# Performance work log

Hardware: AMD Instinct MI355X
Metric: run time of the kernel (lower is better)

The kernel has to match this reference:

```python
import math
import jax, jax.numpy as jnp
import numpy as np

B, L, DIM, HEADS = 4, 2048, 1024, 8
HEAD = DIM // HEADS  # 128
SCALE_BASE = 512.0
EPS = 1e-5  # nn.GroupNorm default


def _xpos(x, downscale=False):
    # x: (..., L, dh). Faithful port of the RetNet XPOS (Jamie-Stirling impl).
    l, dh = x.shape[-2], x.shape[-1]
    half = dh // 2
    pos = jnp.arange(l, dtype=x.dtype)
    base = (jnp.arange(0, dh, 2, dtype=x.dtype) + 0.4 * dh) / (1.4 * dh)  # (half,)
    scale = base[None, :] ** (pos[:, None] / SCALE_BASE)                  # (L, half)
    inv_freq = 1.0 / (10000.0 ** (jnp.arange(half, dtype=x.dtype) / half))
    sinusoid = pos[:, None] * inv_freq[None, :]                           # (L, half)
    sin, cos = jnp.sin(sinusoid), jnp.cos(sinusoid)
    if downscale:
        scale = 1.0 / scale
    s = jnp.repeat(sin * scale, 2, axis=-1)  # duplicate_interleave -> (L, dh)
    c = jnp.repeat(cos * scale, 2, axis=-1)
    x1, x2 = x[..., ::2], x[..., 1::2]
    rot = jnp.stack([-x2, x1], axis=-1).reshape(x.shape)  # rotate_every_two
    return x * c + rot * s


def _decay_mask(l, gammas):
    # D[h, n, m] = gamma_h ** (n - m) for n >= m else 0
    n = jnp.arange(l)[:, None]
    m = jnp.arange(l)[None, :]
    lg = jnp.log(gammas)  # (h,)
    expo = (n - m).astype(jnp.float32)[None, :, :] * lg[:, None, None]
    return jnp.where((n >= m)[None], jnp.exp(expo), 0.0)  # (h, L, L)


def setup_inputs() -> dict:
    key = jax.random.key(0)
    ks = jax.random.split(key, 6)
    d = DIM
    return {
        "X": jax.random.normal(ks[0], (B, L, DIM), dtype=jnp.float32),
        "W_Q": jax.random.normal(ks[1], (HEADS, DIM, HEAD), dtype=jnp.float32) / d,
        "W_K": jax.random.normal(ks[2], (HEADS, DIM, HEAD), dtype=jnp.float32) / d,
        "W_V": jax.random.normal(ks[3], (HEADS, DIM, HEAD), dtype=jnp.float32) / d,
        "W_G": jax.random.normal(ks[4], (DIM, DIM), dtype=jnp.float32) / d,
        "W_O": jax.random.normal(ks[5], (DIM, DIM), dtype=jnp.float32) / d,
        "gn_weight": jnp.ones((DIM,), dtype=jnp.float32),
        "gn_bias": jnp.zeros((DIM,), dtype=jnp.float32),
    }


def reference(X, W_Q, W_K, W_V, W_G, W_O, gn_weight, gn_bias):
    b, l, d = X.shape
    h = W_Q.shape[0]
    # gammas = 1 - exp(linspace(log 1/32, log 1/512, heads))
    gammas = 1.0 - jnp.exp(jnp.linspace(math.log(1.0 / 32.0), math.log(1.0 / 512.0), h)).astype(jnp.float32)

    Q = jnp.einsum('bld,hde->bhle', X, W_Q)
    K = jnp.einsum('bld,hde->bhle', X, W_K)
    V = jnp.einsum('bld,hdv->bhlv', X, W_V)
    Q = _xpos(Q)
    K = _xpos(K, downscale=True)

    D = _decay_mask(l, gammas).astype(X.dtype)           # (h, L, L)
    scores = jnp.einsum('bhle,bhme->bhlm', Q, K) * D[None]
    Y = jnp.einsum('bhlm,bhmv->bhlv', scores, V)          # (b, h, L, head_v)

    # GroupNorm(heads, V) on rows of shape (V,): normalize per head group
    mean = Y.mean(axis=-1, keepdims=True)
    var = Y.var(axis=-1, keepdims=True)
    Yn = (Y - mean) * jax.lax.rsqrt(var + EPS)
    Yn = jnp.transpose(Yn, (0, 2, 1, 3)).reshape(b, l, -1)  # concat heads -> (b, L, V)
    Yn = Yn * gn_weight + gn_bias

    G = X @ W_G
    out = (G * jax.nn.sigmoid(G) * Yn) @ W_O  # swish gate then output proj
    return out
```

## Files before the change

### kernel.cpp

```cpp
#include <hip/hip_runtime.h>
#include <cmath>

#define BB 4
#define LL 2048
#define DD 1024
#define HH 8
#define MM (BB * LL)

struct Gammas { float lg2[8]; };
struct MMArgs { const ushort* Bt[4]; void* C[4]; void* C2[4]; int emode[4]; };

typedef __attribute__((ext_vector_type(8))) short bf16x8;
typedef __attribute__((ext_vector_type(4))) float f32x4;

__device__ __forceinline__ ushort f2bf(float f) {
    uint u = __builtin_bit_cast(uint, f);
    uint r = (u + 0x7fffu + ((u >> 16) & 1u)) >> 16;
    return (ushort)r;
}
__device__ __forceinline__ float bf2f(ushort h) {
    uint u = ((uint)h) << 16;
    return __builtin_bit_cast(float, u);
}
__device__ __forceinline__ void gload16(const void* g, void* l) {
    __builtin_amdgcn_global_load_lds((const __attribute__((address_space(1))) void*)g,
                                     (__attribute__((address_space(3))) void*)l, 16, 0, 0);
}

__global__ void xpos_table_kernel(float4* __restrict__ tbl) {
    int tid = blockIdx.x * blockDim.x + threadIdx.x;
    if (tid >= LL * 64) return;
    int l = tid >> 6, i = tid & 63;
    float inv = powf(10000.0f, -(float)i / 64.0f);
    float ang = (float)l * inv;
    float s = sinf(ang), c = cosf(ang);
    float base = (2.0f * (float)i + 51.2f) / 179.2f;
    float sc = powf(base, (float)l / 512.0f);
    tbl[tid] = make_float4(c * sc, s * sc, c / sc, s / sc);
}

__global__ __launch_bounds__(256) void cast_kernel(const float* __restrict__ X,
                                                   ushort* __restrict__ Xb) {
    int i = (blockIdx.x * 256 + threadIdx.x) * 4;
    float4 v = *(const float4*)&X[i];
    ushort4 o;
    o.x = f2bf(v.x); o.y = f2bf(v.y); o.z = f2bf(v.z); o.w = f2bf(v.w);
    *(ushort4*)&Xb[i] = o;
}

__global__ __launch_bounds__(256) void wtrans_kernel(const float* __restrict__ W,
                                                     ushort* __restrict__ Wt, int perhead) {
    __shared__ float T[64][68];
    const int k0 = blockIdx.y * 64, n0 = blockIdx.x * 64;
    const int t = threadIdx.x;
    for (int f = t; f < 64 * 16; f += 256) {
        int kk = f >> 4, s = f & 15;
        int n = n0 + s * 4;
        size_t src = perhead ? (size_t)(n >> 7) * 131072 + (size_t)(k0 + kk) * 128 + (n & 127)
                             : (size_t)(k0 + kk) * 1024 + n;
        *(float4*)&T[kk][s * 4] = *(const float4*)&W[src];
    }
    __syncthreads();
    for (int f = t; f < 64 * 8; f += 256) {
        int n = f >> 3, s = f & 7;
        __align__(16) ushort tmp[8];
        #pragma unroll
        for (int j = 0; j < 8; j++) tmp[j] = f2bf(T[s * 8 + j][n]);
        *(uint4*)&Wt[(size_t)(n0 + n) * 1024 + k0 + s * 8] = *(uint4*)tmp;
    }
}

#define MM8_STEP(T, STAGE, VM)                                                  \
  {                                                                             \
    const int buf_ = (T) & 3;                                                   \
    const int sbuf_ = ((T) + 2) & 3;                                            \
    if (STAGE) {                                                                \
      const int nk_ = ((T) + 2) * 32;                                           \
      gload16(gA0 + nk_, &As[sbuf_][ldst]);                                     \
      gload16(gA1 + nk_, &As[sbuf_][4096 + ldst]);                              \
    }                                                                           \
    asm volatile("s_waitcnt vmcnt(" #VM ")" ::: "memory");                      \
    __builtin_amdgcn_sched_barrier(0);                                          \
    __builtin_amdgcn_s_barrier();                                               \
    __builtin_amdgcn_sched_barrier(0);                                          \
    bf16x8 am[8], bn[4];                                                        \
    _Pragma("unroll")                                                           \
    for (int mi = 0; mi < 4; mi++)                                              \
      am[mi] = *(const bf16x8*)&As[buf_][aoff + mi * 512];                      \
    _Pragma("unroll")                                                           \
    for (int ni = 0; ni < 4; ni++)                                              \
      bn[ni] = *(const bf16x8*)&Bs[buf_][boff + ni * 512];                      \
    __builtin_amdgcn_s_setprio(1);                                              \
    _Pragma("unroll")                                                           \
    for (int mi = 0; mi < 4; mi++)                                              \
      _Pragma("unroll")                                                         \
      for (int ni = 0; ni < 4; ni++)                                            \
        acc[mi][ni] = __builtin_amdgcn_mfma_f32_16x16x32_bf16(                  \
            am[mi], bn[ni], acc[mi][ni], 0, 0, 0);                              \
    __builtin_amdgcn_s_setprio(0);                                              \
    __builtin_amdgcn_sched_barrier(0);                                          \
    if (STAGE) {                                                                \
      const int nk_ = ((T) + 2) * 32;                                           \
      gload16(gB0 + nk_, &Bs[sbuf_][ldst]);                                     \
      gload16(gB1 + nk_, &Bs[sbuf_][4096 + ldst]);                              \
    }                                                                           \
    __builtin_amdgcn_sched_barrier(0);                                          \
    __builtin_amdgcn_s_barrier();                                               \
    __builtin_amdgcn_sched_barrier(0);                                          \
    _Pragma("unroll")                                                           \
    for (int mi = 4; mi < 8; mi++)                                              \
      am[mi] = *(const bf16x8*)&As[buf_][aoff + mi * 512];                      \
    __builtin_amdgcn_s_setprio(1);                                              \
    _Pragma("unroll")                                                           \
    for (int mi = 4; mi < 8; mi++)                                              \
      _Pragma("unroll")                                                         \
      for (int ni = 0; ni < 4; ni++)                                            \
        acc[mi][ni] = __builtin_amdgcn_mfma_f32_16x16x32_bf16(                  \
            am[mi], bn[ni], acc[mi][ni], 0, 0, 0);                              \
    __builtin_amdgcn_s_setprio(0);                                              \
  }

__global__ __launch_bounds__(512) void mm8_kernel(
    const ushort* __restrict__ A, MMArgs args, const float4* __restrict__ tbl)
{
    __shared__ __align__(16) ushort As[4][8192];
    __shared__ __align__(16) ushort Bs[4][8192];
    const int t = threadIdx.x;
    const int w = t >> 6, lane = t & 63;
    const int ln = lane & 15, quad = lane >> 4;
    const int which = blockIdx.x >> 2;
    const ushort* Bt = args.Bt[which];
    void* Cv = args.C[which];
    void* Cv2 = args.C2[which];
    const int emode = args.emode[which];
    const int n0 = (blockIdx.x & 3) * 256, m0 = blockIdx.y * 256;
    const int wm = w & 1, wn = w >> 1;

    f32x4 acc[8][4];
    const f32x4 fzero = {0.f, 0.f, 0.f, 0.f};
    #pragma unroll
    for (int i = 0; i < 8; i++)
        #pragma unroll
        for (int j = 0; j < 4; j++) acc[i][j] = fzero;

    const int srow = w * 16 + (lane >> 2);
    const int scol = ((lane & 3) ^ ((lane >> 3) & 3)) * 8;
    const ushort* gA0 = A  + (size_t)(m0 + srow) * 1024 + scol;
    const ushort* gA1 = gA0 + (size_t)128 * 1024;
    const ushort* gB0 = Bt + (size_t)(n0 + srow) * 1024 + scol;
    const ushort* gB1 = gB0 + (size_t)128 * 1024;
    const int ldst = w * 512;

    const int cQ = (quad ^ ((ln >> 1) & 3)) * 8;
    const int aoff = (wm * 128 + ln) * 32 + cQ;
    const int boff = (wn * 64 + ln) * 32 + cQ;

    #pragma unroll
    for (int tt = 0; tt < 2; ++tt) {
        gload16(gA0 + tt * 32, &As[tt][ldst]);
        gload16(gA1 + tt * 32, &As[tt][4096 + ldst]);
        gload16(gB0 + tt * 32, &Bs[tt][ldst]);
        gload16(gB1 + tt * 32, &Bs[tt][4096 + ldst]);
    }

    for (int T = 0; T < 30; ++T) {
        MM8_STEP(T, 1, 6);
    }
    MM8_STEP(30, 0, 4);
    MM8_STEP(31, 0, 0);

    #pragma unroll
    for (int mi = 0; mi < 8; mi++) {
        #pragma unroll
        for (int ni = 0; ni < 4; ni++) {
            const int row0 = m0 + wm * 128 + mi * 16 + quad * 4;
            const int e = wn * 64 + ni * 16 + ln;
            const int col = n0 + e;
            if (emode == 5) {
                const int b = row0 >> 11, l0 = row0 & (LL - 1);
                ushort4 pk;
                pk.x = f2bf(acc[mi][ni][0]); pk.y = f2bf(acc[mi][ni][1]);
                pk.z = f2bf(acc[mi][ni][2]); pk.w = f2bf(acc[mi][ni][3]);
                *(ushort4*)&((ushort*)Cv)[((size_t)(b * 1024 + col)) * 2048 + l0] = pk;
                continue;
            }
            float vv[4];
            #pragma unroll
            for (int r = 0; r < 4; r++) {
                float v = acc[mi][ni][r];
                if (emode == 1 || emode == 2 || emode == 6) {
                    float4 tt = tbl[(size_t)((row0 + r) & (LL - 1)) * 64 + ((col & 127) >> 1)];
                    float cc = (emode == 1) ? tt.x : tt.z;
                    float ss = (emode == 1) ? tt.y : tt.w;
                    float partner = __shfl_xor(v, 1);
                    float rot = (col & 1) ? partner : -partner;
                    v = v * cc + rot * ss;
                } else if (emode == 3) {
                    v = v / (1.0f + expf(-v));
                }
                vv[r] = v;
                if (emode == 4)
                    ((float*)Cv)[(size_t)(row0 + r) * 1024 + col] = v;
                else
                    ((ushort*)Cv)[(size_t)(row0 + r) * 1024 + col] = f2bf(v);
            }
            if (emode == 6) {
                const int b = row0 >> 11, l0 = row0 & (LL - 1);
                ushort4 pk;
                pk.x = f2bf(vv[0]); pk.y = f2bf(vv[1]);
                pk.z = f2bf(vv[2]); pk.w = f2bf(vv[3]);
                *(ushort4*)&((ushort*)Cv2)[((size_t)(b * 1024 + col)) * 2048 + l0] = pk;
            }
        }
    }
}

__global__ __launch_bounds__(256) void mm_kernel(
    const ushort* __restrict__ A, MMArgs args, const float4* __restrict__ tbl)
{
    __shared__ __align__(16) ushort As[2][128 * 32];
    __shared__ __align__(16) ushort Bs[2][128 * 32];
    const int t = threadIdx.x;
    const int w = t >> 6, lane = t & 63;
    const int ln = lane & 15, quad = lane >> 4;
    const int which = blockIdx.x >> 3;
    const ushort* Bt = args.Bt[which];
    void* Cv = args.C[which];
    const int emode = args.emode[which];
    const int n0 = (blockIdx.x & 7) * 128, m0 = blockIdx.y * 128;
    const int wm = w & 1, wn = w >> 1;

    f32x4 acc[4][4];
    const f32x4 fzero = {0.f, 0.f, 0.f, 0.f};
    #pragma unroll
    for (int i = 0; i < 4; i++)
        #pragma unroll
        for (int j = 0; j < 4; j++) acc[i][j] = fzero;

    const int srow = w * 32 + (lane >> 2);
    const int scol = (lane & 3) * 8;
    const ushort* ga  = A  + (size_t)(m0 + srow) * 1024 + scol;
    const ushort* ga2 = ga + 16 * 1024;
    const ushort* gb  = Bt + (size_t)(n0 + srow) * 1024 + scol;
    const ushort* gb2 = gb + 16 * 1024;
    const int lo1 = (w * 32) * 32;
    const int lo2 = (w * 32 + 16) * 32;

    gload16(ga, &As[0][lo1]);
    gload16(ga2, &As[0][lo2]);
    gload16(gb, &Bs[0][lo1]);
    gload16(gb2, &Bs[0][lo2]);
    __syncthreads();

    for (int kt = 0; kt < 1024; kt += 32) {
        const int cur = (kt >> 5) & 1;
        if (kt < 1024 - 32) {
            const int nk = kt + 32;
            gload16(ga + nk, &As[cur ^ 1][lo1]);
            gload16(ga2 + nk, &As[cur ^ 1][lo2]);
            gload16(gb + nk, &Bs[cur ^ 1][lo1]);
            gload16(gb2 + nk, &Bs[cur ^ 1][lo2]);
        }
        bf16x8 am[4], bn[4];
        #pragma unroll
        for (int i = 0; i < 4; i++)
            am[i] = *(const bf16x8*)&As[cur][(wm * 64 + i * 16 + ln) * 32 + quad * 8];
        #pragma unroll
        for (int i = 0; i < 4; i++)
            bn[i] = *(const bf16x8*)&Bs[cur][(wn * 64 + i * 16 + ln) * 32 + quad * 8];
        #pragma unroll
        for (int mi = 0; mi < 4; mi++)
            #pragma unroll
            for (int ni = 0; ni < 4; ni++)
                acc[mi][ni] = __builtin_amdgcn_mfma_f32_16x16x32_bf16(
                    am[mi], bn[ni], acc[mi][ni], 0, 0, 0);
        __syncthreads();
    }

    #pragma unroll
    for (int mi = 0; mi < 4; mi++) {
        #pragma unroll
        for (int ni = 0; ni < 4; ni++) {
            const int row0 = m0 + wm * 64 + mi * 16 + quad * 4;
            const int e = wn * 64 + ni * 16 + ln;
            const int col = n0 + e;
            #pragma unroll
            for (int r = 0; r < 4; r++) {
                float v = acc[mi][ni][r];
                if (emode == 3) v = v / (1.0f + expf(-v));
                if (emode == 4)
                    ((float*)Cv)[(size_t)(row0 + r) * 1024 + col] = v;
                else
                    ((ushort*)Cv)[(size_t)(row0 + r) * 1024 + col] = f2bf(v);
            }
        }
    }
}

__global__ __launch_bounds__(256) void state_kernel(
    const ushort* __restrict__ Ktb, const ushort* __restrict__ Vt,
    ushort* __restrict__ Sb, Gammas gp)
{
    __shared__ __align__(16) ushort shbuf[2 * 128 * 72];
    ushort* Ktl = shbuf;
    ushort* Vwl = shbuf + 128 * 72;

    const int t = threadIdx.x;
    const int w = t >> 6, lane = t & 63, ln = lane & 15, quad = lane >> 4;
    const int c = blockIdx.x, bh = blockIdx.y;
    const int b = bh >> 3, h = bh & 7;
    const float lg2 = gp.lg2[h];
    const size_t tbase = ((size_t)b * 1024 + h * 128) * 2048 + (size_t)c * 64;

    const int sr = t >> 1, soff = (t & 1) * 32;
    #pragma unroll
    for (int j = 0; j < 4; j++)
        *(uint4*)&Ktl[sr * 72 + soff + j * 8] =
            *(const uint4*)&Ktb[tbase + (size_t)sr * 2048 + soff + j * 8];
    #pragma unroll
    for (int j = 0; j < 4; j++) {
        uint4 raw = *(const uint4*)&Vt[tbase + (size_t)sr * 2048 + soff + j * 8];
        ushort* rp = (ushort*)&raw;
        __align__(16) ushort tmp[8];
        #pragma unroll
        for (int jj = 0; jj < 8; jj++) {
            int m = soff + j * 8 + jj;
            tmp[jj] = f2bf(bf2f(rp[jj]) * exp2f(lg2 * (float)(63 - m)));
        }
        *(uint4*)&Vwl[sr * 72 + soff + j * 8] = *(uint4*)tmp;
    }
    __syncthreads();

    const int wm = w & 1, wn = w >> 1;
    f32x4 acc[4][4];
    const f32x4 fzero = {0.f, 0.f, 0.f, 0.f};
    #pragma unroll
    for (int i = 0; i < 4; i++)
        #pragma unroll
        for (int j = 0; j < 4; j++) acc[i][j] = fzero;

    #pragma unroll
    for (int ks = 0; ks < 2; ks++) {
        bf16x8 am[4], bn[4];
        #pragma unroll
        for (int mi = 0; mi < 4; mi++)
            am[mi] = *(const bf16x8*)&Ktl[(wm * 64 + mi * 16 + ln) * 72 + ks * 32 + quad * 8];
        #pragma unroll
        for (int ni = 0; ni < 4; ni++)
            bn[ni] = *(const bf16x8*)&Vwl[(wn * 64 + ni * 16 + ln) * 72 + ks * 32 + quad * 8];
        #pragma unroll
        for (int mi = 0; mi < 4; mi++)
            #pragma unroll
            for (int ni = 0; ni < 4; ni++)
                acc[mi][ni] = __builtin_amdgcn_mfma_f32_16x16x32_bf16(
                    am[mi], bn[ni], acc[mi][ni], 0, 0, 0);
    }
    __syncthreads();

    ushort* Lsh = shbuf;
    #pragma unroll
    for (int mi = 0; mi < 4; mi++) {
        #pragma unroll
        for (int ni = 0; ni < 4; ni++) {
            const int d0 = wm * 64 + mi * 16 + quad * 4;
            const int v = wn * 64 + ni * 16 + ln;
            ushort4 pk;
            pk.x = f2bf(acc[mi][ni][0]); pk.y = f2bf(acc[mi][ni][1]);
            pk.z = f2bf(acc[mi][ni][2]); pk.w = f2bf(acc[mi][ni][3]);
            *(ushort4*)&Lsh[v * 136 + d0] = pk;
        }
    }
    __syncthreads();
    ushort* dst = Sb + (size_t)(bh * 32 + c) * 128 * 128;
    const int orow = t >> 1, ooff = (t & 1) * 64;
    #pragma unroll
    for (int j = 0; j < 8; j++)
        *(uint4*)&dst[(size_t)orow * 128 + ooff + j * 8] =
            *(uint4*)&Lsh[orow * 136 + ooff + j * 8];
}

__global__ __launch_bounds__(256) void scan_kernel(ushort* __restrict__ Sb, Gammas gp)
{
    const int t = threadIdx.x;
    const int vb = blockIdx.x, bh = blockIdx.y;
    const int h = bh & 7;
    const float g64 = exp2f(64.0f * gp.lg2[h]);
    const int v = vb * 16 + (t >> 4);
    const int d0 = (t & 15) * 8;

    float acc[8];
    #pragma unroll
    for (int j = 0; j < 8; j++) acc[j] = 0.f;

    for (int c = 1; c < 32; c++) {
        ushort* p = Sb + ((size_t)(bh * 32 + (c - 1)) * 128 + v) * 128 + d0;
        uint4 lv = *(const uint4*)p;
        ushort* lp = (ushort*)&lv;
        __align__(16) ushort o[8];
        #pragma unroll
        for (int j = 0; j < 8; j++) {
            acc[j] = g64 * acc[j] + bf2f(lp[j]);
            o[j] = f2bf(acc[j]);
        }
        *(uint4*)p = *(uint4*)o;
    }
}

__global__ __launch_bounds__(256) void ret2_kernel(
    const ushort* __restrict__ Qb, const ushort* __restrict__ Kb,
    const ushort* __restrict__ Vt, const ushort* __restrict__ Pt,
    const ushort* __restrict__ Gb,
    const float* __restrict__ gnw, const float* __restrict__ gnb,
    ushort* __restrict__ Z, Gammas gp)
{
    __shared__ __align__(16) ushort Ks[64 * 136];
    __shared__ __align__(16) ushort Vs[128 * 72];
    __shared__ __align__(16) ushort Ss[64 * 72];
    __shared__ __align__(16) ushort Ps[128 * 136];

    const int t = threadIdx.x;
    const int w = t >> 6, lane = t & 63, ln = lane & 15, quad = lane >> 4;
    const int c = blockIdx.x, bh = blockIdx.y;
    const int b = bh >> 3, h = bh & 7;
    const float lg2 = gp.lg2[h];
    const size_t qkbase = (size_t)b * LL * 1024 + (size_t)h * 128;
    const size_t vtbase = ((size_t)b * 1024 + h * 128) * 2048;
    const int n0 = c * 64;

    float dmk[4], drr[4];
    #pragma unroll
    for (int kt = 0; kt < 4; kt++)
        dmk[kt] = exp2f(-(float)(kt * 16 + quad * 4) * lg2);
    #pragma unroll
    for (int r = 0; r < 4; r++)
        drr[r] = exp2f(-(float)r * lg2);

    float gwv[8], gbv[8];
    #pragma unroll
    for (int vt = 0; vt < 8; vt++) {
        gwv[vt] = gnw[h * 128 + vt * 16 + ln];
        gbv[vt] = gnb[h * 128 + vt * 16 + ln];
    }

    const int krow = t >> 4, kc = (t & 15) * 8;
    const int vrow = t >> 3, vc = (t & 7) * 8;
    #pragma unroll
    for (int i = 0; i < 4; i++)
        *(uint4*)&Ks[(krow + i * 16) * 136 + kc] =
            *(const uint4*)&Kb[qkbase + (size_t)(n0 + krow + i * 16) * 1024 + kc];
    #pragma unroll
    for (int i = 0; i < 4; i++)
        *(uint4*)&Vs[(vrow + i * 32) * 72 + vc] =
            *(const uint4*)&Vt[vtbase + (size_t)(vrow + i * 32) * 2048 + n0 + vc];
    if (c > 0) {
        const ushort* psrc = Pt + (size_t)(bh * 32 + (c - 1)) * 128 * 128;
        const int pr = t >> 1, poff = (t & 1) * 64;
        #pragma unroll
        for (int j = 0; j < 8; j++)
            *(uint4*)&Ps[pr * 136 + poff + j * 8] =
                *(const uint4*)&psrc[(size_t)pr * 128 + poff + j * 8];
    }

    bf16x8 aq[4];
    #pragma unroll
    for (int ks = 0; ks < 4; ks++)
        aq[ks] = *(const bf16x8*)&Qb[qkbase + (size_t)(n0 + 16 * w + ln) * 1024
                                     + ks * 32 + quad * 8];
    f32x4 y[8];
    const f32x4 fzero = {0.f, 0.f, 0.f, 0.f};
    #pragma unroll
    for (int vt = 0; vt < 8; vt++) y[vt] = fzero;

    __syncthreads();

    if (c > 0) {
        #pragma unroll
        for (int ks = 0; ks < 4; ks++) {
            #pragma unroll
            for (int vt = 0; vt < 8; vt++) {
                bf16x8 bp = *(const bf16x8*)&Ps[(vt * 16 + ln) * 136 + ks * 32 + quad * 8];
                y[vt] = __builtin_amdgcn_mfma_f32_16x16x32_bf16(aq[ks], bp, y[vt], 0, 0, 0);
            }
        }
        #pragma unroll
        for (int rr = 0; rr < 4; rr++) {
            const float sc = exp2f(lg2 * (float)(16 * w + quad * 4 + rr + 1));
            #pragma unroll
            for (int vt = 0; vt < 8; vt++) y[vt][rr] *= sc;
        }
    }

    f32x4 s4[4];
    #pragma unroll
    for (int kt = 0; kt < 4; kt++) s4[kt] = fzero;
    #pragma unroll
    for (int ks = 0; ks < 4; ks++) {
        #pragma unroll
        for (int kt = 0; kt < 4; kt++) {
            bf16x8 bk = *(const bf16x8*)&Ks[(kt * 16 + ln) * 136 + ks * 32 + quad * 8];
            s4[kt] = __builtin_amdgcn_mfma_f32_16x16x32_bf16(bk, aq[ks], s4[kt], 0, 0, 0);
        }
    }
    const float dq = exp2f((float)(16 * w + ln) * lg2);
    #pragma unroll
    for (int kt = 0; kt < 4; kt++) {
        const float db = dq * dmk[kt];
        ushort4 pk;
        pk.x = f2bf((kt * 16 + quad * 4 + 0 <= 16 * w + ln) ? s4[kt][0] * db * drr[0] : 0.f);
        pk.y = f2bf((kt * 16 + quad * 4 + 1 <= 16 * w + ln) ? s4[kt][1] * db * drr[1] : 0.f);
        pk.z = f2bf((kt * 16 + quad * 4 + 2 <= 16 * w + ln) ? s4[kt][2] * db * drr[2] : 0.f);
        pk.w = f2bf((kt * 16 + quad * 4 + 3 <= 16 * w + ln) ? s4[kt][3] * db * drr[3] : 0.f);
        *(ushort4*)&Ss[(16 * w + ln) * 72 + kt * 16 + quad * 4] = pk;
    }
    #pragma unroll
    for (int ks2 = 0; ks2 < 2; ks2++) {
        bf16x8 as = *(const bf16x8*)&Ss[(16 * w + ln) * 72 + ks2 * 32 + quad * 8];
        #pragma unroll
        for (int vt = 0; vt < 8; vt++) {
            bf16x8 bv = *(const bf16x8*)&Vs[(vt * 16 + ln) * 72 + ks2 * 32 + quad * 8];
            y[vt] = __builtin_amdgcn_mfma_f32_16x16x32_bf16(as, bv, y[vt], 0, 0, 0);
        }
    }

    #pragma unroll
    for (int r = 0; r < 4; r++) {
        float s = 0.f, sq = 0.f;
        #pragma unroll
        for (int vt = 0; vt < 8; vt++) {
            float v = y[vt][r];
            s += v; sq += v * v;
        }
        #pragma unroll
        for (int off = 8; off >= 1; off >>= 1) {
            s  += __shfl_xor(s, off, 64);
            sq += __shfl_xor(sq, off, 64);
        }
        float mean = s * 0.0078125f;
        float var = sq * 0.0078125f - mean * mean;
        float rstd = rsqrtf(var + 1e-5f);
        const size_t row = (size_t)(b * LL + n0 + 16 * w + quad * 4 + r);
        #pragma unroll
        for (int vt = 0; vt < 8; vt++) {
            float gv = bf2f(Gb[row * 1024 + h * 128 + vt * 16 + ln]);
            float o = (y[vt][r] - mean) * rstd * gwv[vt] + gbv[vt];
            Z[row * 1024 + h * 128 + vt * 16 + ln] = f2bf(o * gv);
        }
    }
}

extern "C" void kernel_launch(void* const* d_in, const int* in_sizes, int n_in,
                              void* d_out, int out_size, void* d_ws, size_t ws_size,
                              hipStream_t stream) {
    const float* X   = (const float*)d_in[0];
    const float* Wq  = (const float*)d_in[1];
    const float* Wk  = (const float*)d_in[2];
    const float* Wv  = (const float*)d_in[3];
    const float* Wg  = (const float*)d_in[4];
    const float* Wo  = (const float*)d_in[5];
    const float* gnw = (const float*)d_in[6];
    const float* gnb = (const float*)d_in[7];
    float* out = (float*)d_out;

    const size_t MB = 1u << 20;
    char* base = (char*)d_ws;
    ushort* Sb  = (ushort*)base;
    float4* tbl = (float4*)base;
    ushort* Xb  = (ushort*)(base + 2 * MB);
    ushort* Wqt = (ushort*)(base + 18 * MB);
    ushort* Wkt = (ushort*)(base + 20 * MB);
    ushort* Wvt = (ushort*)(base + 22 * MB);
    ushort* Wgt = (ushort*)(base + 24 * MB);
    ushort* Wot = (ushort*)(base + 32 * MB);
    ushort* Qb  = (ushort*)(base + 34 * MB);
    ushort* Kb  = (ushort*)(base + 50 * MB);
    ushort* Gb  = (ushort*)(base + 66 * MB);
    ushort* Vt  = (ushort*)(base + 82 * MB);
    ushort* Ktb = (ushort*)(base + 98 * MB);
    ushort* Zb  = (ushort*)(base + 98 * MB);

    Gammas gp;
    for (int h = 0; h < 8; h++) {
        double lin = log(1.0 / 32.0) +
                     (log(1.0 / 512.0) - log(1.0 / 32.0)) * (double)h / 7.0;
        float gamma = 1.0f - expf((float)lin);
        gp.lg2[h] = log2f(gamma);
    }

    xpos_table_kernel<<<(LL * 64) / 256, 256, 0, stream>>>(tbl);
    cast_kernel<<<MM * 1024 / 1024, 256, 0, stream>>>(X, Xb);

    dim3 wgrid(16, 16);
    wtrans_kernel<<<wgrid, 256, 0, stream>>>(Wq, Wqt, 1);
    wtrans_kernel<<<wgrid, 256, 0, stream>>>(Wk, Wkt, 1);
    wtrans_kernel<<<wgrid, 256, 0, stream>>>(Wv, Wvt, 1);
    wtrans_kernel<<<wgrid, 256, 0, stream>>>(Wg, Wgt, 0);
    wtrans_kernel<<<wgrid, 256, 0, stream>>>(Wo, Wot, 0);

    MMArgs qa;
    qa.Bt[0] = Wqt; qa.Bt[1] = Wkt; qa.Bt[2] = Wvt; qa.Bt[3] = Wgt;
    qa.C[0] = Qb;   qa.C[1] = Kb;   qa.C[2] = Vt;   qa.C[3] = Gb;
    qa.C2[0] = nullptr; qa.C2[1] = Ktb; qa.C2[2] = nullptr; qa.C2[3] = nullptr;
    qa.emode[0] = 1; qa.emode[1] = 6; qa.emode[2] = 5; qa.emode[3] = 3;
    mm8_kernel<<<dim3(16, 32), 512, 0, stream>>>(Xb, qa, tbl);

    state_kernel<<<dim3(32, 32), 256, 0, stream>>>(Ktb, Vt, Sb, gp);
    scan_kernel<<<dim3(8, 32), 256, 0, stream>>>(Sb, gp);
    ret2_kernel<<<dim3(32, 32), 256, 0, stream>>>(Qb, Kb, Vt, Sb, Gb,
                                                  gnw, gnb, Zb, gp);

    MMArgs oa;
    oa.Bt[0] = Wot; oa.Bt[1] = Wot; oa.Bt[2] = Wot; oa.Bt[3] = Wot;
    oa.C[0] = out;  oa.C[1] = out;  oa.C[2] = out;  oa.C[3] = out;
    oa.C2[0] = nullptr; oa.C2[1] = nullptr; oa.C2[2] = nullptr; oa.C2[3] = nullptr;
    oa.emode[0] = 4; oa.emode[1] = 4; oa.emode[2] = 4; oa.emode[3] = 4;
    mm_kernel<<<dim3(8, 64), 256, 0, stream>>>(Zb, oa, tbl);
}
```

Before: 404.5 us.

## Software-pipeline LDS fragment loads across k-steps with one barrier per step

Restructures the mm8 GEMM main loop so the A/B fragments for the next k-tile are read from LDS after the single barrier while the second half of the current MFMAs runs. The upper A half is loaded before the first MFMA group, and B fragments ping-pong between two register sets. This drops one barrier per step and is meant to hide LDS latency behind MFMA work. In exchange it raises register pressure, and the buffer-reuse safety now depends on the 4-deep ring and the vmcnt counts being right.

Result: no change. 404.2 us (-0.1%).

```diff
diff --git a/kernel.cpp b/kernel.cpp
--- a/kernel.cpp
+++ b/kernel.cpp
@@ -70,54 +70,46 @@
     }
 }
 
-#define MM8_STEP(T, STAGE, VM)                                                  \
-  {                                                                             \
-    const int buf_ = (T) & 3;                                                   \
-    const int sbuf_ = ((T) + 2) & 3;                                            \
-    if (STAGE) {                                                                \
-      const int nk_ = ((T) + 2) * 32;                                           \
-      gload16(gA0 + nk_, &As[sbuf_][ldst]);                                     \
-      gload16(gA1 + nk_, &As[sbuf_][4096 + ldst]);                              \
-    }                                                                           \
-    asm volatile("s_waitcnt vmcnt(" #VM ")" ::: "memory");                      \
-    __builtin_amdgcn_sched_barrier(0);                                          \
-    __builtin_amdgcn_s_barrier();                                               \
-    __builtin_amdgcn_sched_barrier(0);                                          \
-    bf16x8 am[8], bn[4];                                                        \
-    _Pragma("unroll")                                                           \
-    for (int mi = 0; mi < 4; mi++)                                              \
-      am[mi] = *(const bf16x8*)&As[buf_][aoff + mi * 512];                      \
-    _Pragma("unroll")                                                           \
-    for (int ni = 0; ni < 4; ni++)                                              \
-      bn[ni] = *(const bf16x8*)&Bs[buf_][boff + ni * 512];                      \
+#define MM8_MFMA(AMV, BNV, OFS)                                                 \
     __builtin_amdgcn_s_setprio(1);                                              \
     _Pragma("unroll")                                                           \
     for (int mi = 0; mi < 4; mi++)                                              \
       _Pragma("unroll")                                                         \
       for (int ni = 0; ni < 4; ni++)                                            \
-        acc[mi][ni] = __builtin_amdgcn_mfma_f32_16x16x32_bf16(                  \
-            am[mi], bn[ni], acc[mi][ni], 0, 0, 0);                              \
-    __builtin_amdgcn_s_setprio(0);                                              \
-    __builtin_amdgcn_sched_barrier(0);                                          \
-    if (STAGE) {                                                                \
+        acc[mi + (OFS)][ni] = __builtin_amdgcn_mfma_f32_16x16x32_bf16(          \
+            AMV[mi], BNV[ni], acc[mi + (OFS)][ni], 0, 0, 0);                    \
+    __builtin_amdgcn_s_setprio(0);
+
+#define MM8_STEP(T, BNC, BNN)                                                   \
+  {                                                                             \
+    const int buf_ = (T) & 3, nbuf_ = ((T) + 1) & 3, sbuf_ = ((T) + 2) & 3;     \
+    if ((T) < 30) {                                                             \
+      const int nk_ = ((T) + 2) * 32;                                           \
+      gload16(gA0 + nk_, &As[sbuf_][ldst]);                                     \
+      gload16(gA1 + nk_, &As[sbuf_][4096 + ldst]);                              \
+    }                                                                           \
+    _Pragma("unroll")                                                           \
+    for (int mi = 0; mi < 4; mi++)                                              \
+      amB[mi] = *(const bf16x8*)&As[buf_][aoff + (mi + 4) * 512];               \
+    MM8_MFMA(amA, BNC, 0)                                                       \
+    if ((T) < 30) {                                                             \
       const int nk_ = ((T) + 2) * 32;                                           \
       gload16(gB0 + nk_, &Bs[sbuf_][ldst]);                                     \
       gload16(gB1 + nk_, &Bs[sbuf_][4096 + ldst]);                              \
     }                                                                           \
-    __builtin_amdgcn_sched_barrier(0);                                          \
+    if ((T) < 30)      asm volatile("s_waitcnt vmcnt(4)" ::: "memory");         \
+    else if ((T) == 30) asm volatile("s_waitcnt vmcnt(0)" ::: "memory");        \
     __builtin_amdgcn_s_barrier();                                               \
     __builtin_amdgcn_sched_barrier(0);                                          \
-    _Pragma("unroll")                                                           \
-    for (int mi = 4; mi < 8; mi++)                                              \
-      am[mi] = *(const bf16x8*)&As[buf_][aoff + mi * 512];                      \
-    __builtin_amdgcn_s_setprio(1);                                              \
-    _Pragma("unroll")                                                           \
-    for (int mi = 4; mi < 8; mi++)                                              \
+    if ((T) < 31) {                                                             \
+      _Pragma("unroll")                                                         \
+      for (int mi = 0; mi < 4; mi++)                                            \
+        amA[mi] = *(const bf16x8*)&As[nbuf_][aoff + mi * 512];                  \
       _Pragma("unroll")                                                         \
       for (int ni = 0; ni < 4; ni++)                                            \
-        acc[mi][ni] = __builtin_amdgcn_mfma_f32_16x16x32_bf16(                  \
-            am[mi], bn[ni], acc[mi][ni], 0, 0, 0);                              \
-    __builtin_amdgcn_s_setprio(0);                                              \
+        BNN[ni] = *(const bf16x8*)&Bs[nbuf_][boff + ni * 512];                  \
+    }                                                                           \
+    MM8_MFMA(amB, BNC, 4)                                                       \
   }
 
 __global__ __launch_bounds__(512) void mm8_kernel(
@@ -155,6 +147,8 @@
     const int aoff = (wm * 128 + ln) * 32 + cQ;
     const int boff = (wn * 64 + ln) * 32 + cQ;
 
+    bf16x8 amA[4], amB[4], bn0[4], bn1[4];
+
     #pragma unroll
     for (int tt = 0; tt < 2; ++tt) {
         gload16(gA0 + tt * 32, &As[tt][ldst]);
@@ -162,12 +156,20 @@
         gload16(gB0 + tt * 32, &Bs[tt][ldst]);
         gload16(gB1 + tt * 32, &Bs[tt][4096 + ldst]);
     }
-
-    for (int T = 0; T < 30; ++T) {
-        MM8_STEP(T, 1, 6);
-    }
-    MM8_STEP(30, 0, 4);
-    MM8_STEP(31, 0, 0);
+    asm volatile("s_waitcnt vmcnt(4)" ::: "memory");
+    __builtin_amdgcn_s_barrier();
+    __builtin_amdgcn_sched_barrier(0);
+    #pragma unroll
+    for (int mi = 0; mi < 4; mi++)
+        amA[mi] = *(const bf16x8*)&As[0][aoff + mi * 512];
+    #pragma unroll
+    for (int ni = 0; ni < 4; ni++)
+        bn0[ni] = *(const bf16x8*)&Bs[0][boff + ni * 512];
+
+    for (int T2 = 0; T2 < 32; T2 += 2) {
+        MM8_STEP(T2,     bn0, bn1)
+        MM8_STEP(T2 + 1, bn1, bn0)
+    }
 
     #pragma unroll
     for (int mi = 0; mi < 8; mi++) {
```
